# Kernel optimization log

Measured on AMD Instinct MI355X. Metric: run time of the kernel, lower is better.

Reference implementation:

```python
import jax, jax.numpy as jnp
import numpy as np

HEADS, DIM_HEAD, DIM = 8, 64, 512
INNER = HEADS * DIM_HEAD  # 512


def setup_inputs() -> dict:
    key = jax.random.key(0)
    k1, k2, k3 = jax.random.split(key, 3)
    b, n = 2, 2048
    x = jax.random.normal(k1, (b, n, DIM), dtype=jnp.float32)
    # to_qkv: Linear(dim, 4*inner_dim, bias=False); weight stored [out, in]
    w_qkv = jax.random.normal(k2, (4 * INNER, DIM), dtype=jnp.float32) * (1.0 / np.sqrt(DIM))
    # to_out: Linear(2*inner_dim, dim) with bias
    w_out = jax.random.normal(k3, (DIM, 2 * INNER), dtype=jnp.float32) * (1.0 / np.sqrt(2 * INNER))
    b_out = jnp.zeros((DIM,), dtype=jnp.float32)
    return {"x": x, "w_qkv": w_qkv, "w_out": w_out, "b_out": b_out}


def reference(x, w_qkv, w_out, b_out):
    b, n, d = x.shape
    qkvt = x @ w_qkv.T  # [b, n, 4*inner]
    q, k, v, t = jnp.split(qkvt, 4, axis=-1)

    def split_heads(z):
        return z.reshape(b, n, HEADS, DIM_HEAD).transpose(0, 2, 1, 3)  # [b,h,n,dh]

    q, k, v, t = map(split_heads, (q, k, v, t))

    scale = DIM_HEAD ** -0.5
    dots = jnp.einsum('bhid,bhjd->bhij', q, k) * scale
    attn1 = jax.nn.softmax(dots, axis=-1)

    # fixed positional-decay attention: exp(-|i-j|/e), torch broadcast-normalized
    idx = jnp.arange(1, n + 1, dtype=x.dtype)  # linspace(1, n, n)
    tg = jnp.abs(idx[None, :] - idx[:, None])  # [n, n]
    a2 = jnp.exp(-tg / jnp.exp(jnp.asarray(1.0, x.dtype)))
    a2 = a2 / a2.sum(-1)  # broadcasts over last axis, as in the torch code

    out1 = jnp.einsum('bhij,bhjd->bhid', attn1, v)
    out2 = jnp.einsum('ij,bhjd->bhid', a2, t)
    out = jnp.concatenate([out1, out2], axis=-1)  # [b,h,n,2*dh]
    out = out.transpose(0, 2, 1, 3).reshape(b, n, HEADS * 2 * DIM_HEAD)  # [b,n,2*inner]
    return out @ w_out.T + b_out
```

## Files before the change

### kernel.cpp

```cpp
#include <hip/hip_runtime.h>
#include <stdint.h>

typedef unsigned short u16;
typedef __bf16 bf16;
typedef __bf16 bf16x8 __attribute__((ext_vector_type(8)));
typedef float f32x4 __attribute__((ext_vector_type(4)));

#define NSEQ 2048
#define NDH 64
#define NH 8
#define QKS 2097152ull

__device__ __forceinline__ float b2f(u16 u) {
  union { float f; uint32_t i; } x; x.i = ((uint32_t)u) << 16; return x.f;
}
__device__ __forceinline__ u16 f2b(float f) {
  union { float f; uint32_t i; } x; x.f = f;
  const uint32_t r = x.i + 0x7FFFu + ((x.i >> 16) & 1u);
  return (u16)(r >> 16);
}

__global__ __launch_bounds__(256) void k_gemm_qkvt(
    const float* __restrict__ X, const float* __restrict__ W, u16* __restrict__ qkvt) {
  __shared__ __align__(16) bf16 smem[18432];
  bf16* As = smem;
  bf16* Bs = smem + 5120;
  const int tid = threadIdx.x;
  const int n0 = blockIdx.x * 128;
  const int m0 = blockIdx.y * 128;
  const int w = tid >> 6, lane = tid & 63;
  const int wy = w >> 1, wx = w & 1;
  const int quad = lane >> 4, l15 = lane & 15;
  const int srow = tid >> 1, shalf = (tid & 1) * 16;
  const float* ax = X + (size_t)(m0 + srow) * 512 + shalf;
  const float* bx = W + (size_t)(n0 + srow) * 512 + shalf;
  f32x4 acc[4][4];
#pragma unroll
  for (int mt = 0; mt < 4; ++mt)
#pragma unroll
    for (int nt = 0; nt < 4; ++nt) acc[mt][nt] = (f32x4){0.f, 0.f, 0.f, 0.f};
  float4 af[4], bf4[4];
#pragma unroll
  for (int p = 0; p < 4; ++p) {
    af[p]  = *(const float4*)(ax + p * 4);
    bf4[p] = *(const float4*)(bx + p * 4);
  }
  for (int kc = 0; kc < 512; kc += 32) {
    __syncthreads();
    {
      u16 ta[8] = {f2b(af[0].x), f2b(af[0].y), f2b(af[0].z), f2b(af[0].w),
                   f2b(af[1].x), f2b(af[1].y), f2b(af[1].z), f2b(af[1].w)};
      u16 tb[8] = {f2b(af[2].x), f2b(af[2].y), f2b(af[2].z), f2b(af[2].w),
                   f2b(af[3].x), f2b(af[3].y), f2b(af[3].z), f2b(af[3].w)};
      *(uint4*)&As[srow * 40 + shalf]     = *(const uint4*)ta;
      *(uint4*)&As[srow * 40 + shalf + 8] = *(const uint4*)tb;
      u16 tc[8] = {f2b(bf4[0].x), f2b(bf4[0].y), f2b(bf4[0].z), f2b(bf4[0].w),
                   f2b(bf4[1].x), f2b(bf4[1].y), f2b(bf4[1].z), f2b(bf4[1].w)};
      u16 td[8] = {f2b(bf4[2].x), f2b(bf4[2].y), f2b(bf4[2].z), f2b(bf4[2].w),
                   f2b(bf4[3].x), f2b(bf4[3].y), f2b(bf4[3].z), f2b(bf4[3].w)};
      *(uint4*)&Bs[srow * 40 + shalf]     = *(const uint4*)tc;
      *(uint4*)&Bs[srow * 40 + shalf + 8] = *(const uint4*)td;
    }
    __syncthreads();
    if (kc + 32 < 512) {
#pragma unroll
      for (int p = 0; p < 4; ++p) {
        af[p]  = *(const float4*)(ax + kc + 32 + p * 4);
        bf4[p] = *(const float4*)(bx + kc + 32 + p * 4);
      }
    }
    bf16x8 afr[4], bfr[4];
#pragma unroll
    for (int mt = 0; mt < 4; ++mt)
      afr[mt] = *(const bf16x8*)&As[(wy * 64 + mt * 16 + l15) * 40 + quad * 8];
#pragma unroll
    for (int nt = 0; nt < 4; ++nt)
      bfr[nt] = *(const bf16x8*)&Bs[(wx * 64 + nt * 16 + l15) * 40 + quad * 8];
#pragma unroll
    for (int mt = 0; mt < 4; ++mt)
#pragma unroll
      for (int nt = 0; nt < 4; ++nt)
        acc[mt][nt] = __builtin_amdgcn_mfma_f32_16x16x32_bf16(afr[mt], bfr[nt], acc[mt][nt], 0, 0, 0);
  }
  __syncthreads();
  const int cbase = n0 + wx * 64;
  const int which = cbase >> 9;
  const int h     = (cbase >> 6) & 7;
  const float scale = (which == 0) ? 0.18033688011112043f : 1.0f;
  bf16* Cw = smem + w * 4608;
  if (which == 2) {
#pragma unroll
    for (int nt = 0; nt < 4; ++nt)
#pragma unroll
      for (int mt = 0; mt < 4; ++mt)
#pragma unroll
        for (int r = 0; r < 4; ++r)
          Cw[(nt * 16 + l15) * 72 + mt * 16 + quad * 4 + r] = (bf16)acc[mt][nt][r];
  } else {
#pragma unroll
    for (int mt = 0; mt < 4; ++mt)
#pragma unroll
      for (int nt = 0; nt < 4; ++nt)
#pragma unroll
        for (int r = 0; r < 4; ++r)
          Cw[(mt * 16 + quad * 4 + r) * 72 + nt * 16 + l15] = (bf16)(acc[mt][nt][r] * scale);
  }
  const int mb = m0 + wy * 64;
  const int bb = mb >> 11;
  const int nn0 = mb & (NSEQ - 1);
  if (which == 2) {
    u16* vt = qkvt + 2ull * QKS + (size_t)(bb * NH + h) * NDH * NSEQ;
#pragma unroll
    for (int p = 0; p < 8; ++p) {
      const int d = p * 8 + (lane >> 3);
      const int t8 = (lane & 7) * 8;
      const uint4 v = *(const uint4*)&Cw[d * 72 + t8];
      *(uint4*)(vt + (size_t)d * NSEQ + nn0 + t8) = v;
    }
  } else {
    u16* dst = qkvt + (size_t)which * QKS + ((size_t)(bb * NH + h) * NSEQ + nn0) * NDH;
#pragma unroll
    for (int p = 0; p < 8; ++p) {
      const int tok = p * 8 + (lane >> 3);
      const int c8 = (lane & 7) * 8;
      const uint4 v = *(const uint4*)&Cw[tok * 72 + c8];
      *(uint4*)(dst + (size_t)tok * NDH + c8) = v;
    }
  }
}

__global__ __launch_bounds__(256) void k_attn(
    const u16* __restrict__ qkvt, u16* __restrict__ out12) {
  __shared__ __align__(16) bf16 Qs[64][72];
  __shared__ __align__(16) bf16 Ks[64][72];
  __shared__ __align__(16) bf16 Vt[64][72];
  __shared__ __align__(16) bf16 Pw[64][76];
  const int tid = threadIdx.x;
  const int bh  = blockIdx.x;
  const int q0  = blockIdx.y * 64;
  const size_t base  = (size_t)bh * (NSEQ * NDH);
  const size_t vbase = 2ull * QKS + (size_t)bh * (NDH * NSEQ);
  const int wq = tid >> 6, lane = tid & 63;
  const int quad = lane >> 4, l15 = lane & 15;
  const int srow = tid >> 2, sc0 = (tid & 3) * 16;
  {
    const u16* qp = qkvt + base + (size_t)(q0 + srow) * NDH + sc0;
    *(uint4*)&Qs[srow][sc0]     = *(const uint4*)qp;
    *(uint4*)&Qs[srow][sc0 + 8] = *(const uint4*)(qp + 8);
  }
  __syncthreads();
  const bf16x8 qa0 = *(const bf16x8*)&Qs[wq * 16 + l15][quad * 8];
  const bf16x8 qa1 = *(const bf16x8*)&Qs[wq * 16 + l15][32 + quad * 8];
  bf16x8 vones;
#pragma unroll
  for (int j = 0; j < 8; ++j) vones[j] = (l15 == 0) ? (bf16)1.f : (bf16)0.f;
  f32x4 lacc = {0.f, 0.f, 0.f, 0.f};
  f32x4 o[4] = {{0.f,0.f,0.f,0.f},{0.f,0.f,0.f,0.f},{0.f,0.f,0.f,0.f},{0.f,0.f,0.f,0.f}};
  const u16* kp = qkvt + QKS + base + (size_t)srow * NDH + sc0;
  const u16* vp = qkvt + vbase + (size_t)srow * NSEQ + sc0;
  uint4 k0 = *(const uint4*)kp;
  uint4 k1 = *(const uint4*)(kp + 8);
  uint4 v0 = *(const uint4*)vp;
  uint4 v1 = *(const uint4*)(vp + 8);
  for (int kt = 0; kt < 32; ++kt) {
    __syncthreads();
    *(uint4*)&Ks[srow][sc0]     = k0;
    *(uint4*)&Ks[srow][sc0 + 8] = k1;
    *(uint4*)&Vt[srow][sc0]     = v0;
    *(uint4*)&Vt[srow][sc0 + 8] = v1;
    __syncthreads();
    if (kt < 31) {
      const u16* kn = kp + (size_t)(kt + 1) * 64 * NDH;
      const u16* vn = vp + (kt + 1) * 64;
      k0 = *(const uint4*)kn;
      k1 = *(const uint4*)(kn + 8);
      v0 = *(const uint4*)vn;
      v1 = *(const uint4*)(vn + 8);
    }
    f32x4 s[4] = {{0.f,0.f,0.f,0.f},{0.f,0.f,0.f,0.f},{0.f,0.f,0.f,0.f},{0.f,0.f,0.f,0.f}};
#pragma unroll
    for (int t = 0; t < 4; ++t) {
      const bf16x8 kb0 = *(const bf16x8*)&Ks[t * 16 + l15][quad * 8];
      const bf16x8 kb1 = *(const bf16x8*)&Ks[t * 16 + l15][32 + quad * 8];
      s[t] = __builtin_amdgcn_mfma_f32_16x16x32_bf16(qa0, kb0, s[t], 0, 0, 0);
      s[t] = __builtin_amdgcn_mfma_f32_16x16x32_bf16(qa1, kb1, s[t], 0, 0, 0);
    }
#pragma unroll
    for (int r = 0; r < 4; ++r) {
      const int prow = wq * 16 + quad * 4 + r;
      Pw[prow][l15]      = (bf16)__builtin_amdgcn_exp2f(s[0][r]);
      Pw[prow][16 + l15] = (bf16)__builtin_amdgcn_exp2f(s[1][r]);
      Pw[prow][32 + l15] = (bf16)__builtin_amdgcn_exp2f(s[2][r]);
      Pw[prow][48 + l15] = (bf16)__builtin_amdgcn_exp2f(s[3][r]);
    }
#pragma unroll
    for (int c = 0; c < 2; ++c) {
      const bf16x8 pa = *(const bf16x8*)&Pw[wq * 16 + l15][c * 32 + quad * 8];
      lacc = __builtin_amdgcn_mfma_f32_16x16x32_bf16(pa, vones, lacc, 0, 0, 0);
#pragma unroll
      for (int nt = 0; nt < 4; ++nt) {
        const bf16x8 vb = *(const bf16x8*)&Vt[nt * 16 + l15][c * 32 + quad * 8];
        o[nt] = __builtin_amdgcn_mfma_f32_16x16x32_bf16(pa, vb, o[nt], 0, 0, 0);
      }
    }
  }
  const int bb = bh >> 3, h = bh & 7;
#pragma unroll
  for (int r = 0; r < 4; ++r) {
    const float lsum = __shfl(lacc[r], lane & 48);
    const float inv = 1.f / lsum;
    const int nn = q0 + wq * 16 + quad * 4 + r;
    u16* dst = out12 + (size_t)(bb * NSEQ + nn) * 1024 + h * 128;
#pragma unroll
    for (int nt = 0; nt < 4; ++nt)
      dst[nt * 16 + l15] = f2b(o[nt][r] * inv);
  }
}

__global__ __launch_bounds__(256) void k_band(
    const u16* __restrict__ qkvt, u16* __restrict__ out12) {
  __shared__ float sinv[4][192];
  __shared__ float fbuf[4][64][68];
  const int tid = threadIdx.x;
  const int w = tid >> 6, d = tid & 63;
  const int c  = blockIdx.x * 4 + w;
  const int i0 = c * 64;
  const int bh = blockIdx.y;
  const size_t tb = 3ull * QKS + (size_t)bh * (NSEQ * NDH);
  const float EI = 0.36787944117144233f;
  const float RR = 0.69220062755534635f;
  const float OMR = 1.f - RR;
#pragma unroll
  for (int p = 0; p < 3; ++p) {
    const int j = i0 - 64 + p * 64 + d;
    const float r1 = __expf(-(float)(j + 1) * EI);
    const float r2 = __expf(-(float)(NSEQ - j) * EI);
    sinv[w][p * 64 + d] = OMR / (1.f - r1 + RR - r2);
  }
  const u16* tp = qkvt + tb + d;
  float f = 0.f;
  if (c > 0) {
#pragma unroll 8
    for (int jj = 0; jj < 64; ++jj)
      f = RR * f + sinv[w][jj] * b2f(tp[(size_t)(i0 - 64 + jj) * NDH]);
  }
#pragma unroll 8
  for (int jj = 0; jj < 64; ++jj) {
    f = RR * f + sinv[w][64 + jj] * b2f(tp[(size_t)(i0 + jj) * NDH]);
    fbuf[w][jj][d] = f;
  }
  float b = 0.f;
  if (c < 31) {
#pragma unroll 8
    for (int jj = 63; jj >= 0; --jj)
      b = RR * b + sinv[w][128 + jj] * b2f(tp[(size_t)(i0 + 64 + jj) * NDH]);
  }
  const int bb = bh >> 3, h = bh & 7;
#pragma unroll 8
  for (int jj = 63; jj >= 0; --jj) {
    const float g = sinv[w][64 + jj] * b2f(tp[(size_t)(i0 + jj) * NDH]);
    b = RR * b + g;
    out12[(size_t)(bb * NSEQ + i0 + jj) * 1024 + h * 128 + 64 + d] =
        f2b(fbuf[w][jj][d] + b - g);
  }
}

__global__ __launch_bounds__(256) void k_gemm_out(
    const u16* __restrict__ A, const float* __restrict__ W,
    const float* __restrict__ bias, float* __restrict__ out) {
  __shared__ __align__(16) float smemf[4352];
  bf16* As = (bf16*)smemf;
  bf16* Bs = (bf16*)smemf + 2560;
  const int tid = threadIdx.x;
  const int n0 = blockIdx.x * 64;
  const int m0 = blockIdx.y * 64;
  const int w = tid >> 6, lane = tid & 63;
  const int quad = lane >> 4, l15 = lane & 15;
  const int srow = tid >> 2, scol = (tid & 3) * 8;
  const u16*   ap = A + (size_t)(m0 + srow) * 1024 + scol;
  const float* bp = W + (size_t)(n0 + srow) * 1024 + scol;
  f32x4 acc[4];
#pragma unroll
  for (int nt = 0; nt < 4; ++nt) acc[nt] = (f32x4){0.f, 0.f, 0.f, 0.f};
  uint4 a0 = *(const uint4*)ap;
  float4 b0 = *(const float4*)bp;
  float4 b1 = *(const float4*)(bp + 4);
  for (int kc = 0; kc < 1024; kc += 32) {
    __syncthreads();
    *(uint4*)&As[srow * 40 + scol] = a0;
    {
      u16 tb[8] = {f2b(b0.x), f2b(b0.y), f2b(b0.z), f2b(b0.w),
                   f2b(b1.x), f2b(b1.y), f2b(b1.z), f2b(b1.w)};
      *(uint4*)&Bs[srow * 40 + scol] = *(const uint4*)tb;
    }
    __syncthreads();
    if (kc + 32 < 1024) {
      a0 = *(const uint4*)(ap + kc + 32);
      b0 = *(const float4*)(bp + kc + 32);
      b1 = *(const float4*)(bp + kc + 36);
    }
    const bf16x8 af = *(const bf16x8*)&As[(w * 16 + l15) * 40 + quad * 8];
#pragma unroll
    for (int nt = 0; nt < 4; ++nt) {
      const bf16x8 bfr = *(const bf16x8*)&Bs[(nt * 16 + l15) * 40 + quad * 8];
      acc[nt] = __builtin_amdgcn_mfma_f32_16x16x32_bf16(af, bfr, acc[nt], 0, 0, 0);
    }
  }
  float bias_v[4];
#pragma unroll
  for (int nt = 0; nt < 4; ++nt) bias_v[nt] = bias[n0 + nt * 16 + l15];
  __syncthreads();
  float* Cw = smemf + w * 1088;
#pragma unroll
  for (int nt = 0; nt < 4; ++nt)
#pragma unroll
    for (int r = 0; r < 4; ++r)
      Cw[(quad * 4 + r) * 68 + nt * 16 + l15] = acc[nt][r] + bias_v[nt];
#pragma unroll
  for (int p = 0; p < 4; ++p) {
    const int row = p * 4 + (lane >> 4);
    const int c4  = (lane & 15) * 4;
    const float4 v = *(const float4*)&Cw[row * 68 + c4];
    *(float4*)(out + (size_t)(m0 + w * 16 + row) * 512 + n0 + c4) = v;
  }
}

extern "C" void kernel_launch(void* const* d_in, const int* in_sizes, int n_in,
                              void* d_out, int out_size, void* d_ws, size_t ws_size,
                              hipStream_t stream) {
  (void)in_sizes; (void)n_in; (void)out_size; (void)ws_size;
  const float* x     = (const float*)d_in[0];
  const float* w_qkv = (const float*)d_in[1];
  const float* w_out = (const float*)d_in[2];
  const float* b_out = (const float*)d_in[3];
  float* out = (float*)d_out;
  u16* qkvt  = (u16*)d_ws;
  u16* out12 = (u16*)d_ws + 8ull * 1024 * 1024;
  k_gemm_qkvt<<<dim3(16, 32), 256, 0, stream>>>(x, w_qkv, qkvt);
  k_attn     <<<dim3(16, 32), 256, 0, stream>>>(qkvt, out12);
  k_band     <<<dim3(8, 16), 256, 0, stream>>>(qkvt, out12);
  k_gemm_out <<<dim3(8, 64), 256, 0, stream>>>(out12, w_out, b_out, out);
}
```

Baseline: 160.4 us.

## Use 32x32x16 MFMA in attention with split-K waves and packed bf16 conversion

The attention kernel moves from 16x16 MFMA tiles to 32x32x16 MFMA tiles. The four waves become a 2x2 grid over query halves and key halves, each computing transposed scores (K times Q), and the two key-half partial outputs and row sums are combined through shared memory at the end. Row sums now come from summing the exponentials in registers instead of an extra MFMA against a ones vector. The GEMM kernels also swap per-element manual bf16 rounding for packed float2-to-bf16x2 conversion intrinsics, which cuts ALU work in the staging path, at the cost of an extra reduction step and more shared memory.

Measured after the change: 149.6 us. -6.8%, faster.

```diff
diff --git a/kernel.cpp b/kernel.cpp
--- a/kernel.cpp
+++ b/kernel.cpp
@@ -1,10 +1,12 @@
 #include <hip/hip_runtime.h>
+#include <hip/hip_bf16.h>
 #include <stdint.h>
 
 typedef unsigned short u16;
 typedef __bf16 bf16;
 typedef __bf16 bf16x8 __attribute__((ext_vector_type(8)));
 typedef float f32x4 __attribute__((ext_vector_type(4)));
+typedef float f32x16 __attribute__((ext_vector_type(16)));
 
 #define NSEQ 2048
 #define NDH 64
@@ -18,6 +20,11 @@
   union { float f; uint32_t i; } x; x.f = f;
   const uint32_t r = x.i + 0x7FFFu + ((x.i >> 16) & 1u);
   return (u16)(r >> 16);
+}
+__device__ __forceinline__ uint32_t b2pk(float a, float b) {
+  union { __hip_bfloat162 h; uint32_t u; } x;
+  x.h = __float22bfloat162_rn(make_float2(a, b));
+  return x.u;
 }
 
 __global__ __launch_bounds__(256) void k_gemm_qkvt(
@@ -48,18 +55,18 @@
   for (int kc = 0; kc < 512; kc += 32) {
     __syncthreads();
     {
-      u16 ta[8] = {f2b(af[0].x), f2b(af[0].y), f2b(af[0].z), f2b(af[0].w),
-                   f2b(af[1].x), f2b(af[1].y), f2b(af[1].z), f2b(af[1].w)};
-      u16 tb[8] = {f2b(af[2].x), f2b(af[2].y), f2b(af[2].z), f2b(af[2].w),
-                   f2b(af[3].x), f2b(af[3].y), f2b(af[3].z), f2b(af[3].w)};
-      *(uint4*)&As[srow * 40 + shalf]     = *(const uint4*)ta;
-      *(uint4*)&As[srow * 40 + shalf + 8] = *(const uint4*)tb;
-      u16 tc[8] = {f2b(bf4[0].x), f2b(bf4[0].y), f2b(bf4[0].z), f2b(bf4[0].w),
-                   f2b(bf4[1].x), f2b(bf4[1].y), f2b(bf4[1].z), f2b(bf4[1].w)};
-      u16 td[8] = {f2b(bf4[2].x), f2b(bf4[2].y), f2b(bf4[2].z), f2b(bf4[2].w),
-                   f2b(bf4[3].x), f2b(bf4[3].y), f2b(bf4[3].z), f2b(bf4[3].w)};
-      *(uint4*)&Bs[srow * 40 + shalf]     = *(const uint4*)tc;
-      *(uint4*)&Bs[srow * 40 + shalf + 8] = *(const uint4*)td;
+      uint4 ta = {b2pk(af[0].x, af[0].y), b2pk(af[0].z, af[0].w),
+                  b2pk(af[1].x, af[1].y), b2pk(af[1].z, af[1].w)};
+      uint4 tb = {b2pk(af[2].x, af[2].y), b2pk(af[2].z, af[2].w),
+                  b2pk(af[3].x, af[3].y), b2pk(af[3].z, af[3].w)};
+      *(uint4*)&As[srow * 40 + shalf]     = ta;
+      *(uint4*)&As[srow * 40 + shalf + 8] = tb;
+      uint4 tc = {b2pk(bf4[0].x, bf4[0].y), b2pk(bf4[0].z, bf4[0].w),
+                  b2pk(bf4[1].x, bf4[1].y), b2pk(bf4[1].z, bf4[1].w)};
+      uint4 td = {b2pk(bf4[2].x, bf4[2].y), b2pk(bf4[2].z, bf4[2].w),
+                  b2pk(bf4[3].x, bf4[3].y), b2pk(bf4[3].z, bf4[3].w)};
+      *(uint4*)&Bs[srow * 40 + shalf]     = tc;
+      *(uint4*)&Bs[srow * 40 + shalf + 8] = td;
     }
     __syncthreads();
     if (kc + 32 < 512) {
@@ -131,31 +138,37 @@
 
 __global__ __launch_bounds__(256) void k_attn(
     const u16* __restrict__ qkvt, u16* __restrict__ out12) {
-  __shared__ __align__(16) bf16 Qs[64][72];
-  __shared__ __align__(16) bf16 Ks[64][72];
-  __shared__ __align__(16) bf16 Vt[64][72];
-  __shared__ __align__(16) bf16 Pw[64][76];
+  __shared__ __align__(16) bf16 Qs[64 * 72];
+  __shared__ __align__(16) bf16 KV[2 * 64 * 72];
+  __shared__ __align__(16) bf16 Pw[4 * 32 * 72];
+  __shared__ float Lpart[4][32];
+  bf16* Ks = KV;
+  bf16* Vt = KV + 64 * 72;
   const int tid = threadIdx.x;
   const int bh  = blockIdx.x;
   const int q0  = blockIdx.y * 64;
   const size_t base  = (size_t)bh * (NSEQ * NDH);
   const size_t vbase = 2ull * QKS + (size_t)bh * (NDH * NSEQ);
   const int wq = tid >> 6, lane = tid & 63;
-  const int quad = lane >> 4, l15 = lane & 15;
+  const int qh = wq >> 1, kh = wq & 1;
+  const int l31 = lane & 31, hi = lane >> 5;
   const int srow = tid >> 2, sc0 = (tid & 3) * 16;
   {
     const u16* qp = qkvt + base + (size_t)(q0 + srow) * NDH + sc0;
-    *(uint4*)&Qs[srow][sc0]     = *(const uint4*)qp;
-    *(uint4*)&Qs[srow][sc0 + 8] = *(const uint4*)(qp + 8);
-  }
-  __syncthreads();
-  const bf16x8 qa0 = *(const bf16x8*)&Qs[wq * 16 + l15][quad * 8];
-  const bf16x8 qa1 = *(const bf16x8*)&Qs[wq * 16 + l15][32 + quad * 8];
-  bf16x8 vones;
-#pragma unroll
-  for (int j = 0; j < 8; ++j) vones[j] = (l15 == 0) ? (bf16)1.f : (bf16)0.f;
-  f32x4 lacc = {0.f, 0.f, 0.f, 0.f};
-  f32x4 o[4] = {{0.f,0.f,0.f,0.f},{0.f,0.f,0.f,0.f},{0.f,0.f,0.f,0.f},{0.f,0.f,0.f,0.f}};
+    *(uint4*)&Qs[srow * 72 + sc0]     = *(const uint4*)qp;
+    *(uint4*)&Qs[srow * 72 + sc0 + 8] = *(const uint4*)(qp + 8);
+  }
+  __syncthreads();
+  bf16x8 qb[4];
+#pragma unroll
+  for (int c = 0; c < 4; ++c)
+    qb[c] = *(const bf16x8*)&Qs[(qh * 32 + l31) * 72 + c * 16 + hi * 8];
+  float lacc = 0.f;
+  f32x16 o[2];
+#pragma unroll
+  for (int nt = 0; nt < 2; ++nt)
+#pragma unroll
+    for (int r = 0; r < 16; ++r) o[nt][r] = 0.f;
   const u16* kp = qkvt + QKS + base + (size_t)srow * NDH + sc0;
   const u16* vp = qkvt + vbase + (size_t)srow * NSEQ + sc0;
   uint4 k0 = *(const uint4*)kp;
@@ -164,10 +177,10 @@
   uint4 v1 = *(const uint4*)(vp + 8);
   for (int kt = 0; kt < 32; ++kt) {
     __syncthreads();
-    *(uint4*)&Ks[srow][sc0]     = k0;
-    *(uint4*)&Ks[srow][sc0 + 8] = k1;
-    *(uint4*)&Vt[srow][sc0]     = v0;
-    *(uint4*)&Vt[srow][sc0 + 8] = v1;
+    *(uint4*)&Ks[srow * 72 + sc0]     = k0;
+    *(uint4*)&Ks[srow * 72 + sc0 + 8] = k1;
+    *(uint4*)&Vt[srow * 72 + sc0]     = v0;
+    *(uint4*)&Vt[srow * 72 + sc0 + 8] = v1;
     __syncthreads();
     if (kt < 31) {
       const u16* kn = kp + (size_t)(kt + 1) * 64 * NDH;
@@ -177,43 +190,63 @@
       v0 = *(const uint4*)vn;
       v1 = *(const uint4*)(vn + 8);
     }
-    f32x4 s[4] = {{0.f,0.f,0.f,0.f},{0.f,0.f,0.f,0.f},{0.f,0.f,0.f,0.f},{0.f,0.f,0.f,0.f}};
-#pragma unroll
-    for (int t = 0; t < 4; ++t) {
-      const bf16x8 kb0 = *(const bf16x8*)&Ks[t * 16 + l15][quad * 8];
-      const bf16x8 kb1 = *(const bf16x8*)&Ks[t * 16 + l15][32 + quad * 8];
-      s[t] = __builtin_amdgcn_mfma_f32_16x16x32_bf16(qa0, kb0, s[t], 0, 0, 0);
-      s[t] = __builtin_amdgcn_mfma_f32_16x16x32_bf16(qa1, kb1, s[t], 0, 0, 0);
-    }
-#pragma unroll
-    for (int r = 0; r < 4; ++r) {
-      const int prow = wq * 16 + quad * 4 + r;
-      Pw[prow][l15]      = (bf16)__builtin_amdgcn_exp2f(s[0][r]);
-      Pw[prow][16 + l15] = (bf16)__builtin_amdgcn_exp2f(s[1][r]);
-      Pw[prow][32 + l15] = (bf16)__builtin_amdgcn_exp2f(s[2][r]);
-      Pw[prow][48 + l15] = (bf16)__builtin_amdgcn_exp2f(s[3][r]);
+    f32x16 s;
+#pragma unroll
+    for (int r = 0; r < 16; ++r) s[r] = 0.f;
+#pragma unroll
+    for (int c = 0; c < 4; ++c) {
+      const bf16x8 ka = *(const bf16x8*)&Ks[(kh * 32 + l31) * 72 + c * 16 + hi * 8];
+      s = __builtin_amdgcn_mfma_f32_32x32x16_bf16(ka, qb[c], s, 0, 0, 0);
+    }
+    float ts = 0.f;
+#pragma unroll
+    for (int r = 0; r < 16; ++r) {
+      s[r] = __builtin_amdgcn_exp2f(s[r]);
+      ts += s[r];
+    }
+    ts += __shfl_xor(ts, 32);
+    lacc += ts;
+    bf16* pr = Pw + (wq * 32 + l31) * 72;
+#pragma unroll
+    for (int g = 0; g < 4; ++g) {
+      bf16 pk[4] = {(bf16)s[4 * g], (bf16)s[4 * g + 1],
+                    (bf16)s[4 * g + 2], (bf16)s[4 * g + 3]};
+      *(uint2*)&pr[g * 8 + hi * 4] = *(const uint2*)pk;
     }
 #pragma unroll
     for (int c = 0; c < 2; ++c) {
-      const bf16x8 pa = *(const bf16x8*)&Pw[wq * 16 + l15][c * 32 + quad * 8];
-      lacc = __builtin_amdgcn_mfma_f32_16x16x32_bf16(pa, vones, lacc, 0, 0, 0);
-#pragma unroll
-      for (int nt = 0; nt < 4; ++nt) {
-        const bf16x8 vb = *(const bf16x8*)&Vt[nt * 16 + l15][c * 32 + quad * 8];
-        o[nt] = __builtin_amdgcn_mfma_f32_16x16x32_bf16(pa, vb, o[nt], 0, 0, 0);
+      const bf16x8 pa = *(const bf16x8*)&Pw[(wq * 32 + l31) * 72 + c * 16 + hi * 8];
+      const bf16x8 vb0 = *(const bf16x8*)&Vt[l31 * 72 + kh * 32 + c * 16 + hi * 8];
+      const bf16x8 vb1 = *(const bf16x8*)&Vt[(32 + l31) * 72 + kh * 32 + c * 16 + hi * 8];
+      o[0] = __builtin_amdgcn_mfma_f32_32x32x16_bf16(pa, vb0, o[0], 0, 0, 0);
+      o[1] = __builtin_amdgcn_mfma_f32_32x32x16_bf16(pa, vb1, o[1], 0, 0, 0);
+    }
+  }
+  __syncthreads();
+  if (lane < 32) Lpart[wq][lane] = lacc;
+  float* Osum = (float*)KV;
+  if (kh == 1) {
+#pragma unroll
+    for (int nt = 0; nt < 2; ++nt)
+#pragma unroll
+      for (int r = 0; r < 16; ++r) {
+        const int row = (r & 3) + 8 * (r >> 2) + 4 * hi;
+        Osum[(qh * 32 + row) * 64 + nt * 32 + l31] = o[nt][r];
       }
-    }
-  }
-  const int bb = bh >> 3, h = bh & 7;
-#pragma unroll
-  for (int r = 0; r < 4; ++r) {
-    const float lsum = __shfl(lacc[r], lane & 48);
-    const float inv = 1.f / lsum;
-    const int nn = q0 + wq * 16 + quad * 4 + r;
-    u16* dst = out12 + (size_t)(bb * NSEQ + nn) * 1024 + h * 128;
-#pragma unroll
-    for (int nt = 0; nt < 4; ++nt)
-      dst[nt * 16 + l15] = f2b(o[nt][r] * inv);
+  }
+  __syncthreads();
+  if (kh == 0) {
+    const int bb = bh >> 3, h = bh & 7;
+#pragma unroll
+    for (int r = 0; r < 16; ++r) {
+      const int row = (r & 3) + 8 * (r >> 2) + 4 * hi;
+      const float lt = Lpart[qh * 2][row] + Lpart[qh * 2 + 1][row];
+      const float inv = 1.f / lt;
+      const int nn = q0 + qh * 32 + row;
+      u16* dst = out12 + (size_t)(bb * NSEQ + nn) * 1024 + h * 128;
+      dst[l31]      = f2b((o[0][r] + Osum[(qh * 32 + row) * 64 + l31]) * inv);
+      dst[32 + l31] = f2b((o[1][r] + Osum[(qh * 32 + row) * 64 + 32 + l31]) * inv);
+    }
   }
 }
 
@@ -289,9 +322,9 @@
     __syncthreads();
     *(uint4*)&As[srow * 40 + scol] = a0;
     {
-      u16 tb[8] = {f2b(b0.x), f2b(b0.y), f2b(b0.z), f2b(b0.w),
-                   f2b(b1.x), f2b(b1.y), f2b(b1.z), f2b(b1.w)};
-      *(uint4*)&Bs[srow * 40 + scol] = *(const uint4*)tb;
+      uint4 tb = {b2pk(b0.x, b0.y), b2pk(b0.z, b0.w),
+                  b2pk(b1.x, b1.y), b2pk(b1.z, b1.w)};
+      *(uint4*)&Bs[srow * 40 + scol] = tb;
     }
     __syncthreads();
     if (kc + 32 < 1024) {
```
